# Kernel tuning notes

Measured on AMD Instinct MI355X. Metric: run time of the kernel, lower is better.

The kernel has to match this reference:

```python
import jax, jax.numpy as jnp
import numpy as np

K = 7          # kernel_size
PAD = 3        # padding (same-size output)
GROUPS = 8


def _unfold(z, H, W):
    # z: [B, C, H+2p, W+2p] -> patches [B, C, H, W, K*K], flat index = kh*K + kw
    # matches torch .unfold(2,K,1).unfold(3,K,1).view(..., -1)
    return jnp.stack(
        [z[:, :, a:a + H, b:b + W] for a in range(K) for b in range(K)],
        axis=-1,
    )


def setup_inputs() -> dict:
    key = jax.random.key(0)
    ks = jax.random.split(key, 7)
    B, C, H, W = 4, 64, 64, 64
    Cout = 64
    fan_scale = (2.0 / Cout) ** 0.5  # kaiming fan_out, 1x1 conv
    return {
        "x": jax.random.normal(ks[0], (B, C, H, W), jnp.float32),
        "y": jax.random.normal(ks[1], (B, C, H, W), jnp.float32),
        "Wq": jax.random.normal(ks[2], (Cout, C), jnp.float32) * fan_scale,
        "Wk": jax.random.normal(ks[3], (Cout, C), jnp.float32) * fan_scale,
        "Wv": jax.random.normal(ks[4], (Cout, C), jnp.float32) * fan_scale,
        "rel_h": jax.random.normal(ks[5], (Cout // 2, K), jnp.float32),
        "rel_w": jax.random.normal(ks[6], (Cout // 2, K), jnp.float32),
    }


def reference(x, y, Wq, Wk, Wv, rel_h, rel_w):
    B, C, H, W = x.shape
    Cout = Wq.shape[0]
    half = Cout // 2

    # 1x1 convs (no bias) commute with zero padding, so project first.
    q = jnp.einsum('oc,bchw->bohw', Wq, x)          # [B, Cout, H, W]
    k_full = jnp.einsum('oc,bchw->bohw', Wk, x)
    v_full = jnp.einsum('oc,bchw->bohw', Wv, y)

    pad4 = ((0, 0), (0, 0), (PAD, PAD), (PAD, PAD))
    k_pat = _unfold(jnp.pad(k_full, pad4), H, W)    # [B, Cout, H, W, K*K]
    v_pat = _unfold(jnp.pad(v_full, pad4), H, W)

    # relative-position bias: rel_h over kh (top half of channels), rel_w over kw
    bias_h = jnp.broadcast_to(rel_h[:, :, None], (half, K, K))   # [Cout/2, kh, kw]
    bias_w = jnp.broadcast_to(rel_w[:, None, :], (half, K, K))
    bias = jnp.concatenate([bias_h, bias_w], axis=0).reshape(Cout, K * K)
    k_pat = k_pat + bias[None, :, None, None, :]

    cg = Cout // GROUPS
    k_pat = k_pat.reshape(B, GROUPS, cg, H, W, K * K)
    v_pat = v_pat.reshape(B, GROUPS, cg, H, W, K * K)
    q = q.reshape(B, GROUPS, cg, H, W, 1)

    attn = jax.nn.softmax(q * k_pat, axis=-1)       # per-channel softmax over window
    out = jnp.sum(attn * v_pat, axis=-1)            # [B, G, cg, H, W]
    return out.reshape(B, Cout, H, W)
```

## Files before the change

kernel.cpp:

```cpp
#include <hip/hip_runtime.h>

#define HW 4096

typedef float f4 __attribute__((ext_vector_type(4)));
typedef float f2 __attribute__((ext_vector_type(2)));

#define WSTRIDE 194

__global__ __launch_bounds__(256) void proj_kernel(
    const float* __restrict__ x, const float* __restrict__ y,
    const float* __restrict__ Wq, const float* __restrict__ Wk,
    const float* __restrict__ Wv,
    float* __restrict__ q, float* __restrict__ k, float* __restrict__ v)
{
    __shared__ float wlds[64 * WSTRIDE];
    const int t = threadIdx.x;

    {
        const float* Ws[3] = {Wq, Wk, Wv};
#pragma unroll
        for (int m = 0; m < 3; ++m) {
#pragma unroll
            for (int s = 0; s < 4; ++s) {
                const int fi = s * 256 + t;
                const int co = fi >> 4, c4 = fi & 15;
                const f4 w = *(const f4*)&Ws[m][co * 64 + c4 * 4];
#pragma unroll
                for (int i = 0; i < 4; ++i)
                    wlds[(c4 * 4 + i) * WSTRIDE + m * 64 + co] = w[i];
            }
        }
    }
    __syncthreads();

    const int cg  = t & 31;
    const int pq  = t >> 5;
    const int px0 = blockIdx.x * 64;
    const int b   = px0 >> 12;
    const int poff = (px0 & 4095) + pq * 8;
    const float* xb = x + (size_t)b * 64 * HW + poff;
    const float* yb = y + (size_t)b * 64 * HW + poff;

    f4 acc[3][2][2];
#pragma unroll
    for (int m = 0; m < 3; ++m)
#pragma unroll
        for (int i = 0; i < 2; ++i)
#pragma unroll
            for (int h = 0; h < 2; ++h)
                acc[m][i][h] = (f4){0.f, 0.f, 0.f, 0.f};

#pragma unroll 4
    for (int c = 0; c < 64; ++c) {
        const f4 xv0 = *(const f4*)&xb[c * HW];
        const f4 xv1 = *(const f4*)&xb[c * HW + 4];
        const f4 yv0 = *(const f4*)&yb[c * HW];
        const f4 yv1 = *(const f4*)&yb[c * HW + 4];
        const float* wr = &wlds[c * WSTRIDE + 2 * cg];
        const f2 wq = *(const f2*)&wr[0];
        const f2 wk = *(const f2*)&wr[64];
        const f2 wv = *(const f2*)&wr[128];
        acc[0][0][0] += xv0 * wq[0];  acc[0][0][1] += xv1 * wq[0];
        acc[0][1][0] += xv0 * wq[1];  acc[0][1][1] += xv1 * wq[1];
        acc[1][0][0] += xv0 * wk[0];  acc[1][0][1] += xv1 * wk[0];
        acc[1][1][0] += xv0 * wk[1];  acc[1][1][1] += xv1 * wk[1];
        acc[2][0][0] += yv0 * wv[0];  acc[2][0][1] += yv1 * wv[0];
        acc[2][1][0] += yv0 * wv[1];  acc[2][1][1] += yv1 * wv[1];
    }

    {
        float* outs[3] = {q, k, v};
#pragma unroll
        for (int m = 0; m < 3; ++m)
#pragma unroll
            for (int i = 0; i < 2; ++i) {
                float* dst = outs[m] + ((size_t)b * 64 + 2 * cg + i) * HW + poff;
                *(f4*)&dst[0] = acc[m][i][0];
                *(f4*)&dst[4] = acc[m][i][1];
            }
    }
}

__global__ __launch_bounds__(256) void attn_kernel(
    const float* __restrict__ qg, const float* __restrict__ kg,
    const float* __restrict__ vg,
    const float* __restrict__ rel_h, const float* __restrict__ rel_w,
    float* __restrict__ out)
{
    __shared__ float kT[22 * 72];
    __shared__ float vT[22 * 72];

    const int blk = blockIdx.x;
    const int bc  = blk >> 2;
    const int h0  = (blk & 3) << 4;
    const int c   = bc & 63;
    const int t   = threadIdx.x;

    const float* kimg = kg + (size_t)bc * HW;
    const float* vimg = vg + (size_t)bc * HW;
    const f4 z4 = {0.f, 0.f, 0.f, 0.f};

    if (t < 88) {
        const int row = t >> 2, side = (t >> 1) & 1, arr = t & 1;
        float* dst = arr ? vT : kT;
        *(f4*)&dst[row * 72 + side * 68] = z4;
    }
#pragma unroll
    for (int j = 0; j < 2; ++j) {
        const int idx = j * 256 + t;
        if (idx < 352) {
            const int row = idx >> 4, ch = idx & 15;
            const int hy = h0 - 3 + row;
            const bool rv = ((unsigned)hy < 64u);
            const f4 kv = rv ? *(const f4*)&kimg[hy * 64 + ch * 4] : z4;
            const f4 vv = rv ? *(const f4*)&vimg[hy * 64 + ch * 4] : z4;
            *(f4*)&kT[row * 72 + ch * 4 + 4] = kv;
            *(f4*)&vT[row * 72 + ch * 4 + 4] = vv;
        }
    }
    __syncthreads();

    const int r  = t >> 4;
    const int w0 = (t & 15) << 2;
    const int h  = h0 + r;

    const float LOG2E = 1.4426950408889634f;
    const f4 qv = *(const f4*)&qg[(size_t)bc * HW + h * 64 + w0];
    float qe[4];
#pragma unroll
    for (int p = 0; p < 4; ++p) qe[p] = qv[p] * LOG2E;

    float bh[7], bw[7];
    if (c < 32) {
#pragma unroll
        for (int a = 0; a < 7; ++a) { bh[a] = rel_h[c * 7 + a]; bw[a] = 0.f; }
    } else {
#pragma unroll
        for (int a = 0; a < 7; ++a) { bh[a] = 0.f; bw[a] = rel_w[(c - 32) * 7 + a]; }
    }

    float l[4] = {0.f, 0.f, 0.f, 0.f};
    float o[4] = {0.f, 0.f, 0.f, 0.f};

#pragma unroll
    for (int a = 0; a < 7; ++a) {
        const int ro = (r + a) * 72 + w0;
        const f4 k0 = *(const f4*)&kT[ro];
        const f4 k1 = *(const f4*)&kT[ro + 4];
        const f4 k2 = *(const f4*)&kT[ro + 8];
        const f4 v0 = *(const f4*)&vT[ro];
        const f4 v1 = *(const f4*)&vT[ro + 4];
        const f4 v2 = *(const f4*)&vT[ro + 8];
        const float kw[12] = {k0[0], k0[1], k0[2], k0[3], k1[0], k1[1], k1[2], k1[3],
                              k2[0], k2[1], k2[2], k2[3]};
        const float vw[12] = {v0[0], v0[1], v0[2], v0[3], v1[0], v1[1], v1[2], v1[3],
                              v2[0], v2[1], v2[2], v2[3]};
        const float bha = bh[a];
#pragma unroll
        for (int b2 = 0; b2 < 7; ++b2) {
            const float bias = bha + bw[b2];
#pragma unroll
            for (int p = 0; p < 4; ++p) {
                float s = qe[p] * (kw[p + b2 + 1] + bias);
                s = fminf(s, 115.f);
                const float e = __builtin_amdgcn_exp2f(s);
                l[p] += e;
                o[p] = fmaf(e, vw[p + b2 + 1], o[p]);
            }
        }
    }

    f4 res;
#pragma unroll
    for (int p = 0; p < 4; ++p)
        res[p] = o[p] * __builtin_amdgcn_rcpf(l[p]);
    *(f4*)&out[(size_t)bc * HW + h * 64 + w0] = res;
}

extern "C" void kernel_launch(void* const* d_in, const int* in_sizes, int n_in,
                              void* d_out, int out_size, void* d_ws, size_t ws_size,
                              hipStream_t stream) {
    const float* x   = (const float*)d_in[0];
    const float* y   = (const float*)d_in[1];
    const float* Wq  = (const float*)d_in[2];
    const float* Wk  = (const float*)d_in[3];
    const float* Wv  = (const float*)d_in[4];
    const float* rlh = (const float*)d_in[5];
    const float* rlw = (const float*)d_in[6];
    float* out = (float*)d_out;

    float* q = (float*)d_ws;
    float* k = q + (1 << 20);
    float* v = k + (1 << 20);

    proj_kernel<<<256, 256, 0, stream>>>(x, y, Wq, Wk, Wv, q, k, v);
    attn_kernel<<<1024, 256, 0, stream>>>(q, k, v, rlh, rlw, out);
}
```

Measured before the change: 97.68 us.

## Stage projection outputs through LDS and precompute q*bias in attention

The projection kernel now writes its accumulators into a swizzled LDS tile and then stores them back as fully coalesced 64-float rows, rather than scattering 8-float segments per thread. Its channel loop unroll also goes from 4 to 8. The attention kernel precomputes q*bias per row or column and specialises the loop for the rel_h and rel_w channel halves, so each score is a single FMA. It also drops the fminf clamp before exp2, which assumes the scores cannot overflow.

```diff
diff --git a/kernel.cpp b/kernel.cpp
--- a/kernel.cpp
+++ b/kernel.cpp
@@ -11,9 +11,9 @@
     const float* __restrict__ x, const float* __restrict__ y,
     const float* __restrict__ Wq, const float* __restrict__ Wk,
     const float* __restrict__ Wv,
-    float* __restrict__ q, float* __restrict__ k, float* __restrict__ v)
+    float* __restrict__ qkv)
 {
-    __shared__ float wlds[64 * WSTRIDE];
+    __shared__ float lds[64 * WSTRIDE];
     const int t = threadIdx.x;
 
     {
@@ -27,7 +27,7 @@
                 const f4 w = *(const f4*)&Ws[m][co * 64 + c4 * 4];
 #pragma unroll
                 for (int i = 0; i < 4; ++i)
-                    wlds[(c4 * 4 + i) * WSTRIDE + m * 64 + co] = w[i];
+                    lds[(c4 * 4 + i) * WSTRIDE + m * 64 + co] = w[i];
             }
         }
     }
@@ -37,7 +37,8 @@
     const int pq  = t >> 5;
     const int px0 = blockIdx.x * 64;
     const int b   = px0 >> 12;
-    const int poff = (px0 & 4095) + pq * 8;
+    const int poffb = px0 & 4095;
+    const int poff  = poffb + pq * 8;
     const float* xb = x + (size_t)b * 64 * HW + poff;
     const float* yb = y + (size_t)b * 64 * HW + poff;
 
@@ -50,13 +51,13 @@
             for (int h = 0; h < 2; ++h)
                 acc[m][i][h] = (f4){0.f, 0.f, 0.f, 0.f};
 
-#pragma unroll 4
+#pragma unroll 8
     for (int c = 0; c < 64; ++c) {
         const f4 xv0 = *(const f4*)&xb[c * HW];
         const f4 xv1 = *(const f4*)&xb[c * HW + 4];
         const f4 yv0 = *(const f4*)&yb[c * HW];
         const f4 yv1 = *(const f4*)&yb[c * HW + 4];
-        const float* wr = &wlds[c * WSTRIDE + 2 * cg];
+        const float* wr = &lds[c * WSTRIDE + 2 * cg];
         const f2 wq = *(const f2*)&wr[0];
         const f2 wk = *(const f2*)&wr[64];
         const f2 wv = *(const f2*)&wr[128];
@@ -68,16 +69,28 @@
         acc[2][1][0] += yv0 * wv[1];  acc[2][1][1] += yv1 * wv[1];
     }
 
-    {
-        float* outs[3] = {q, k, v};
-#pragma unroll
-        for (int m = 0; m < 3; ++m)
-#pragma unroll
-            for (int i = 0; i < 2; ++i) {
-                float* dst = outs[m] + ((size_t)b * 64 + 2 * cg + i) * HW + poff;
-                *(f4*)&dst[0] = acc[m][i][0];
-                *(f4*)&dst[4] = acc[m][i][1];
+    __syncthreads();
+
+#pragma unroll
+    for (int m = 0; m < 3; ++m)
+#pragma unroll
+        for (int i = 0; i < 2; ++i)
+#pragma unroll
+            for (int h = 0; h < 2; ++h) {
+                const int row = m * 64 + 2 * cg + i;
+                const int ch  = pq * 2 + h;
+                *(f4*)&lds[row * 64 + ((ch ^ (row & 15)) << 2)] = acc[m][i][h];
             }
+    __syncthreads();
+
+#pragma unroll
+    for (int s = 0; s < 12; ++s) {
+        const int fi  = s * 256 + t;
+        const int row = fi >> 4, ch = fi & 15;
+        const f4 val = *(const f4*)&lds[row * 64 + ((ch ^ (row & 15)) << 2)];
+        float* dst = qkv + (size_t)(row >> 6) * (1 << 20)
+                         + ((size_t)b * 64 + (row & 63)) * HW + poffb + ch * 4;
+        *(f4*)dst = val;
     }
 }
 
@@ -130,43 +143,73 @@
 #pragma unroll
     for (int p = 0; p < 4; ++p) qe[p] = qv[p] * LOG2E;
 
-    float bh[7], bw[7];
+    float qb[7][4];
     if (c < 32) {
 #pragma unroll
-        for (int a = 0; a < 7; ++a) { bh[a] = rel_h[c * 7 + a]; bw[a] = 0.f; }
+        for (int a = 0; a < 7; ++a) {
+            const float bb = rel_h[c * 7 + a];
+#pragma unroll
+            for (int p = 0; p < 4; ++p) qb[a][p] = qe[p] * bb;
+        }
     } else {
 #pragma unroll
-        for (int a = 0; a < 7; ++a) { bh[a] = 0.f; bw[a] = rel_w[(c - 32) * 7 + a]; }
+        for (int j = 0; j < 7; ++j) {
+            const float bb = rel_w[(c - 32) * 7 + j];
+#pragma unroll
+            for (int p = 0; p < 4; ++p) qb[j][p] = qe[p] * bb;
+        }
     }
 
     float l[4] = {0.f, 0.f, 0.f, 0.f};
     float o[4] = {0.f, 0.f, 0.f, 0.f};
 
-#pragma unroll
-    for (int a = 0; a < 7; ++a) {
-        const int ro = (r + a) * 72 + w0;
-        const f4 k0 = *(const f4*)&kT[ro];
-        const f4 k1 = *(const f4*)&kT[ro + 4];
-        const f4 k2 = *(const f4*)&kT[ro + 8];
-        const f4 v0 = *(const f4*)&vT[ro];
-        const f4 v1 = *(const f4*)&vT[ro + 4];
-        const f4 v2 = *(const f4*)&vT[ro + 8];
-        const float kw[12] = {k0[0], k0[1], k0[2], k0[3], k1[0], k1[1], k1[2], k1[3],
-                              k2[0], k2[1], k2[2], k2[3]};
-        const float vw[12] = {v0[0], v0[1], v0[2], v0[3], v1[0], v1[1], v1[2], v1[3],
-                              v2[0], v2[1], v2[2], v2[3]};
-        const float bha = bh[a];
-#pragma unroll
-        for (int b2 = 0; b2 < 7; ++b2) {
-            const float bias = bha + bw[b2];
-#pragma unroll
-            for (int p = 0; p < 4; ++p) {
-                float s = qe[p] * (kw[p + b2 + 1] + bias);
-                s = fminf(s, 115.f);
-                const float e = __builtin_amdgcn_exp2f(s);
-                l[p] += e;
-                o[p] = fmaf(e, vw[p + b2 + 1], o[p]);
-            }
+    if (c < 32) {
+#pragma unroll
+        for (int a = 0; a < 7; ++a) {
+            const int ro = (r + a) * 72 + w0;
+            const f4 k0 = *(const f4*)&kT[ro];
+            const f4 k1 = *(const f4*)&kT[ro + 4];
+            const f4 k2 = *(const f4*)&kT[ro + 8];
+            const f4 v0 = *(const f4*)&vT[ro];
+            const f4 v1 = *(const f4*)&vT[ro + 4];
+            const f4 v2 = *(const f4*)&vT[ro + 8];
+            const float kw[12] = {k0[0], k0[1], k0[2], k0[3], k1[0], k1[1], k1[2], k1[3],
+                                  k2[0], k2[1], k2[2], k2[3]};
+            const float vw[12] = {v0[0], v0[1], v0[2], v0[3], v1[0], v1[1], v1[2], v1[3],
+                                  v2[0], v2[1], v2[2], v2[3]};
+#pragma unroll
+            for (int b2 = 0; b2 < 7; ++b2)
+#pragma unroll
+                for (int p = 0; p < 4; ++p) {
+                    const float s = fmaf(qe[p], kw[p + b2 + 1], qb[a][p]);
+                    const float e = __builtin_amdgcn_exp2f(s);
+                    l[p] += e;
+                    o[p] = fmaf(e, vw[p + b2 + 1], o[p]);
+                }
+        }
+    } else {
+#pragma unroll
+        for (int a = 0; a < 7; ++a) {
+            const int ro = (r + a) * 72 + w0;
+            const f4 k0 = *(const f4*)&kT[ro];
+            const f4 k1 = *(const f4*)&kT[ro + 4];
+            const f4 k2 = *(const f4*)&kT[ro + 8];
+            const f4 v0 = *(const f4*)&vT[ro];
+            const f4 v1 = *(const f4*)&vT[ro + 4];
+            const f4 v2 = *(const f4*)&vT[ro + 8];
+            const float kw[12] = {k0[0], k0[1], k0[2], k0[3], k1[0], k1[1], k1[2], k1[3],
+                                  k2[0], k2[1], k2[2], k2[3]};
+            const float vw[12] = {v0[0], v0[1], v0[2], v0[3], v1[0], v1[1], v1[2], v1[3],
+                                  v2[0], v2[1], v2[2], v2[3]};
+#pragma unroll
+            for (int b2 = 0; b2 < 7; ++b2)
+#pragma unroll
+                for (int p = 0; p < 4; ++p) {
+                    const float s = fmaf(qe[p], kw[p + b2 + 1], qb[b2][p]);
+                    const float e = __builtin_amdgcn_exp2f(s);
+                    l[p] += e;
+                    o[p] = fmaf(e, vw[p + b2 + 1], o[p]);
+                }
         }
     }
 
@@ -189,10 +232,11 @@
     const float* rlw = (const float*)d_in[6];
     float* out = (float*)d_out;
 
-    float* q = (float*)d_ws;
-    float* k = q + (1 << 20);
-    float* v = k + (1 << 20);
-
-    proj_kernel<<<256, 256, 0, stream>>>(x, y, Wq, Wk, Wv, q, k, v);
+    float* qkv = (float*)d_ws;
+    float* q = qkv;
+    float* k = qkv + (1 << 20);
+    float* v = qkv + (2 << 20);
+
+    proj_kernel<<<256, 256, 0, stream>>>(x, y, Wq, Wk, Wv, qkv);
     attn_kernel<<<1024, 256, 0, stream>>>(q, k, v, rlh, rlw, out);
 }
```

Result: slower. 106.1 us (+8.6%).
